# Performance work log

Measured on AMD Instinct MI355X. Metric: run time of the kernel, lower is better.

Reference implementation:

```python
import jax, jax.numpy as jnp
import numpy as np

B, F, D, K = 4096, 1, 256, 65536

def setup_inputs() -> dict:
    key = jax.random.key(0)
    k1, k2, k3 = jax.random.split(key, 3)
    xhat_BFD = jax.random.normal(k1, (B, F, D), dtype=jnp.float32)
    x_BD = jax.random.normal(k2, (B * F, D), dtype=jnp.float32)
    centroids = jax.random.normal(k3, (K, D), dtype=jnp.float32)
    return {"xhat_BFD": xhat_BFD, "x_BD": x_BD, "centroids": centroids}

def reference(xhat_BFD, x_BD, centroids):
    c_sq_K = jnp.sum(centroids * centroids, axis=-1)            # [K]
    dists_BK = c_sq_K[None, :] - 2.0 * (x_BD @ centroids.T)     # [B*F, K] (GEMM-based distances)
    codes_B = jnp.argmin(dists_BK, axis=-1)                      # [B*F]
    quant_x_BD = centroids[codes_B]                              # embedding lookup of winners
    Bb, Ff, Dd = xhat_BFD.shape
    xhat_next = quant_x_BD.reshape(Bb, Ff, Dd)
    codes_BF = codes_B.reshape(Bb, Ff)
    return xhat_next, codes_BF
```

## Files before the change

### kernel.cpp

```cpp
#include <hip/hip_runtime.h>
#include <hip/hip_bf16.h>
#include <math.h>


#define DDIM 256
#define QTILE 128
#define STSZ 8192
#define QCAP 48
#define F16_MINN 6.103515625e-5f

typedef __attribute__((ext_vector_type(8))) _Float16 half8;
typedef __attribute__((ext_vector_type(4))) _Float16 half4;
typedef __attribute__((ext_vector_type(4))) float f32x4;

__device__ __forceinline__ void gl_lds16(const void* g, void* l) {
  __builtin_amdgcn_global_load_lds((const __attribute__((address_space(1))) void*)g,
                                   (__attribute__((address_space(3))) void*)l, 16, 0, 0);
}

__device__ __forceinline__ unsigned fkey(float d) {
  unsigned ud = __float_as_uint(d);
  return ud ^ (((int)ud < 0) ? 0xFFFFFFFFu : 0x80000000u);
}

__global__ void initctl_kernel(unsigned* __restrict__ ctl) {
  if (threadIdx.x < 64) ctl[threadIdx.x] = 0u;
}

__global__ __launch_bounds__(256) void splitc_kernel(const float* __restrict__ in,
                                                     _Float16* __restrict__ o0,
                                                     float* __restrict__ c_sq) {
  int i = blockIdx.x * 256 + threadIdx.x;
  int lane = (int)threadIdx.x & 63;
  float4 v = ((const float4*)in)[i];
  float vv[4] = {v.x, v.y, v.z, v.w};
  half4 h0;
#pragma unroll
  for (int e = 0; e < 4; ++e)
    h0[e] = (fabsf(vv[e]) < F16_MINN) ? (_Float16)0.f : (_Float16)vv[e];
  *(half4*)(o0 + (size_t)i * 4) = h0;
  float s = fmaf(v.x, v.x, fmaf(v.y, v.y, fmaf(v.z, v.z, v.w * v.w)));
#pragma unroll
  for (int off = 32; off > 0; off >>= 1) s += __shfl_down(s, off, 64);
  if (lane == 0) c_sq[i >> 6] = s;
}

__global__ __launch_bounds__(256) void splitx_kernel(const float* __restrict__ in,
                                                     _Float16* __restrict__ o0, int n4) {
  int i = blockIdx.x * 256 + threadIdx.x;
  if (i >= n4) return;
  float4 v = ((const float4*)in)[i];
  float vv[4] = {v.x, v.y, v.z, v.w};
  half4 h0;
#pragma unroll
  for (int e = 0; e < 4; ++e)
    h0[e] = (fabsf(vv[e]) < F16_MINN) ? (_Float16)0.f : (_Float16)vv[e];
  *(half4*)(o0 + (size_t)i * 4) = h0;
}

__global__ __launch_bounds__(256) void cmax_kernel(const float* __restrict__ c_sq,
                                                   unsigned* __restrict__ ctl) {
  __shared__ float red[4];
  int t = blockIdx.x * 256 + (int)threadIdx.x;
  float4 v = ((const float4*)c_sq)[t];
  float m = fmaxf(fmaxf(v.x, v.y), fmaxf(v.z, v.w));
#pragma unroll
  for (int off = 32; off > 0; off >>= 1) m = fmaxf(m, __shfl_down(m, off, 64));
  int lane = (int)threadIdx.x & 63, w = (int)threadIdx.x >> 6;
  if (lane == 0) red[w] = m;
  __syncthreads();
  if (threadIdx.x == 0) {
    m = fmaxf(fmaxf(red[0], red[1]), fmaxf(red[2], red[3]));
    atomicMax(&ctl[32], __float_as_uint(m));
  }
}

__global__ __launch_bounds__(1024) void scan_kernel(
    const _Float16* __restrict__ x0, const _Float16* __restrict__ c0,
    const float* __restrict__ c_sq, float* __restrict__ dm) {
  __shared__ __align__(16) _Float16 As0[32768];

  const int kc = blockIdx.x, qb = blockIdx.y;
  const int tid = (int)threadIdx.x;
  const int lane = tid & 63, w = tid >> 6;
  const int col = lane & 15, quad = lane >> 4;
  const int qrow0 = qb * QTILE;

#pragma unroll
  for (int i = 0; i < 4; ++i) {
    int u = i * 1024 + tid;
    int q = u & 127, s = u >> 7;
    gl_lds16(x0 + (size_t)(qrow0 + q) * DDIM + s * 8, As0 + (size_t)u * 8);
  }
  __syncthreads();

  for (int ct = 0; ct < STSZ / 512; ++ct) {
    const int cbase = kc * STSZ + ct * 512 + w * 32;
    f32x4 acc[2][8];
#pragma unroll
    for (int cm = 0; cm < 2; ++cm)
#pragma unroll
      for (int qn = 0; qn < 8; ++qn) acc[cm][qn] = (f32x4)0.0f;

#pragma unroll 2
    for (int kt = 0; kt < 8; ++kt) {
      const int k0 = kt * 32;
      half8 cf[2];
#pragma unroll
      for (int cm = 0; cm < 2; ++cm)
        cf[cm] = *(const half8*)(c0 + (size_t)(cbase + cm * 16 + col) * DDIM + k0 + quad * 8);
#pragma unroll
      for (int qn = 0; qn < 8; ++qn) {
        half8 qf = *(const half8*)(As0 + (size_t)(((kt * 4 + quad) * QTILE) + qn * 16 + col) * 8);
#pragma unroll
        for (int cm = 0; cm < 2; ++cm)
          acc[cm][qn] = __builtin_amdgcn_mfma_f32_16x16x32_f16(cf[cm], qf, acc[cm][qn], 0, 0, 0);
      }
    }

    f32x4 csv[2];
#pragma unroll
    for (int cm = 0; cm < 2; ++cm)
      csv[cm] = *(const f32x4*)(c_sq + cbase + cm * 16 + quad * 4);
    const int grp = kc * (STSZ / 32) + ct * 16 + w;
    float* dmg = dm + (size_t)grp * 4096 + qrow0;
#pragma unroll
    for (int qn = 0; qn < 8; ++qn) {
      float mq = INFINITY;
#pragma unroll
      for (int cm = 0; cm < 2; ++cm)
#pragma unroll
        for (int rg = 0; rg < 4; ++rg)
          mq = fminf(mq, fmaf(-2.0f, acc[cm][qn][rg], csv[cm][rg]));
      mq = fminf(mq, __shfl_xor(mq, 16, 64));
      mq = fminf(mq, __shfl_xor(mq, 32, 64));
      if (quad == 0) dmg[qn * 16 + col] = mq;
    }
  }
}

__global__ __launch_bounds__(256) void pmin_kernel(const float* __restrict__ dm,
                                                   float* __restrict__ pm) {
  int qc = blockIdx.x & 15, gc = blockIdx.x >> 4;
  int q = qc * 256 + (int)threadIdx.x;
  float m = INFINITY;
  for (int g = gc * 128; g < gc * 128 + 128; ++g)
    m = fminf(m, dm[(size_t)g * 4096 + q]);
  pm[gc * 4096 + q] = m;
}

__global__ __launch_bounds__(256) void tq_kernel(const float* __restrict__ pm,
                                                 const float* __restrict__ x,
                                                 const unsigned* __restrict__ ctl,
                                                 float* __restrict__ T,
                                                 unsigned* __restrict__ cnt) {
  int q = blockIdx.x * 256 + (int)threadIdx.x;
  float M = INFINITY;
#pragma unroll
  for (int i = 0; i < 16; ++i) M = fminf(M, pm[i * 4096 + q]);
  float xsq = 0.f;
  const float4* xr = (const float4*)(x + (size_t)q * DDIM);
#pragma unroll 8
  for (int i = 0; i < 64; ++i) {
    float4 v = xr[i];
    xsq = fmaf(v.x, v.x, fmaf(v.y, v.y, fmaf(v.z, v.z, fmaf(v.w, v.w, xsq))));
  }
  float cmaxsq = __uint_as_float(ctl[32]);
  T[q] = M + 0.0078125f * sqrtf(xsq * cmaxsq) + 1.0f;
  cnt[q] = 0u;
}

__global__ __launch_bounds__(256) void emit_kernel(const float* __restrict__ dm,
                                                   const float* __restrict__ T,
                                                   unsigned short* __restrict__ cand,
                                                   unsigned* __restrict__ cnt) {
  int qc = blockIdx.x & 15, gc = blockIdx.x >> 4;
  int q = qc * 256 + (int)threadIdx.x;
  float t = T[q];
  for (int g = gc * 128; g < gc * 128 + 128; ++g)
    if (dm[(size_t)g * 4096 + q] <= t) {
      unsigned slot = atomicAdd(&cnt[q], 1u);
      if (slot < QCAP) cand[(size_t)q * QCAP + slot] = (unsigned short)g;
    }
}

__global__ __launch_bounds__(256) void rescore_final_kernel(
    const unsigned short* __restrict__ cand, const unsigned* __restrict__ cnt,
    const float* __restrict__ x, const float* __restrict__ cent,
    const float* __restrict__ c_sq, float* __restrict__ out) {
  int q = blockIdx.x * 4 + ((int)threadIdx.x >> 6);
  int lane = (int)threadIdx.x & 63;
  unsigned n = cnt[q];
  unsigned long long best = 0xFFFFFFFFFFFFFFFFull;
  if (n >= 1 && n <= QCAP) {
    int dh = (lane & 1) * 128;
    const float4* xr = (const float4*)(x + (size_t)q * DDIM + dh);
    for (unsigned sl = 0; sl < n; ++sl) {
      int g = (int)cand[(size_t)q * QCAP + sl];
      int c = g * 32 + (lane >> 1);
      const float4* cr = (const float4*)(cent + (size_t)c * DDIM + dh);
      float s = 0.f;
#pragma unroll
      for (int i = 0; i < 32; ++i) {
        float4 a = xr[i], bb = cr[i];
        s = fmaf(a.x, bb.x, fmaf(a.y, bb.y, fmaf(a.z, bb.z, fmaf(a.w, bb.w, s))));
      }
      s += __shfl_xor(s, 1, 64);
      float d = (lane & 1) ? INFINITY : fmaf(-2.0f, s, c_sq[c]);
      unsigned long long pkv = ((unsigned long long)fkey(d) << 32) | (unsigned)c;
      if (pkv < best) best = pkv;
    }
  } else {
    const float4* xr = (const float4*)(x + (size_t)q * DDIM);
    for (int c = lane; c < 65536; c += 64) {
      const float4* cr = (const float4*)(cent + (size_t)c * DDIM);
      float s = 0.f;
#pragma unroll 16
      for (int i = 0; i < 64; ++i) {
        float4 a = xr[i], bb = cr[i];
        s = fmaf(a.x, bb.x, fmaf(a.y, bb.y, fmaf(a.z, bb.z, fmaf(a.w, bb.w, s))));
      }
      float d = fmaf(-2.0f, s, c_sq[c]);
      unsigned long long pkv = ((unsigned long long)fkey(d) << 32) | (unsigned)c;
      if (pkv < best) best = pkv;
    }
  }
#pragma unroll
  for (int off = 1; off < 64; off <<= 1) {
    unsigned long long o = __shfl_xor(best, off, 64);
    if (o < best) best = o;
  }
  int idx = (int)(unsigned)(best & 0xFFFFFFFFu);
  float4 v = ((const float4*)cent)[(size_t)idx * 64 + lane];
  ((float4*)out)[(size_t)q * 64 + lane] = v;
  if (lane == 0) out[(size_t)4096 * DDIM + q] = (float)idx;
}

extern "C" void kernel_launch(void* const* d_in, const int* in_sizes, int n_in,
                              void* d_out, int out_size, void* d_ws, size_t ws_size,
                              hipStream_t stream) {
  const float* x    = (const float*)d_in[1];
  const float* cent = (const float*)d_in[2];
  float* out = (float*)d_out;
  char* ws = (char*)d_ws;

  const size_t OFF_C0   = 0;
  const size_t OFF_X0   = 33554432;
  const size_t OFF_CSQ  = 35651584;
  const size_t OFF_CTL  = 35913728;
  const size_t OFF_DM   = 35913984;
  const size_t OFF_PM   = 69468416;
  const size_t OFF_T    = 69730560;
  const size_t OFF_CNT  = 69746944;
  const size_t OFF_CAND = 69763328;
  const size_t NEED     = 72089600;
  if (ws_size < NEED) return;

  _Float16* c0 = (_Float16*)(ws + OFF_C0);
  _Float16* x0 = (_Float16*)(ws + OFF_X0);
  float* c_sq = (float*)(ws + OFF_CSQ);
  unsigned* ctl = (unsigned*)(ws + OFF_CTL);
  float* dm = (float*)(ws + OFF_DM);
  float* pm = (float*)(ws + OFF_PM);
  float* T  = (float*)(ws + OFF_T);
  unsigned* cnt = (unsigned*)(ws + OFF_CNT);
  unsigned short* cand = (unsigned short*)(ws + OFF_CAND);

  initctl_kernel<<<1, 64, 0, stream>>>(ctl);
  splitc_kernel<<<16384, 256, 0, stream>>>(cent, c0, c_sq);
  splitx_kernel<<<1024, 256, 0, stream>>>(x, x0, 4096 * 256 / 4);
  cmax_kernel<<<64, 256, 0, stream>>>(c_sq, ctl);
  scan_kernel<<<dim3(8, 32), 1024, 0, stream>>>(x0, c0, c_sq, dm);
  pmin_kernel<<<256, 256, 0, stream>>>(dm, pm);
  tq_kernel<<<16, 256, 0, stream>>>(pm, x, ctl, T, cnt);
  emit_kernel<<<256, 256, 0, stream>>>(dm, T, cand, cnt);
  rescore_final_kernel<<<1024, 256, 0, stream>>>(cand, cnt, x, cent, c_sq, out);
}
```

Measured before the change: 380.1 us.

## Fuse per-tile min into scan, fold init into splitx, widen rescore to block-per-query

Drops the separate initctl and pmin launches: the control-word reset moves into splitx, and each scan block now keeps a shared-memory running minimum per query and writes one partial minimum per centroid chunk (8 chunks instead of 16). The rescore kernel now assigns a whole 256-thread block to each query, splitting candidates across four waves and combining them through shared memory. This saves two launches and the full re-read of the distance matrix, and gives rescore four times the parallelism, at the cost of extra LDS work in the scan epilogue.

```diff
diff --git a/kernel.cpp b/kernel.cpp
--- a/kernel.cpp
+++ b/kernel.cpp
@@ -21,10 +21,6 @@
 __device__ __forceinline__ unsigned fkey(float d) {
   unsigned ud = __float_as_uint(d);
   return ud ^ (((int)ud < 0) ? 0xFFFFFFFFu : 0x80000000u);
-}
-
-__global__ void initctl_kernel(unsigned* __restrict__ ctl) {
-  if (threadIdx.x < 64) ctl[threadIdx.x] = 0u;
 }
 
 __global__ __launch_bounds__(256) void splitc_kernel(const float* __restrict__ in,
@@ -46,7 +42,9 @@
 }
 
 __global__ __launch_bounds__(256) void splitx_kernel(const float* __restrict__ in,
-                                                     _Float16* __restrict__ o0, int n4) {
+                                                     _Float16* __restrict__ o0, int n4,
+                                                     unsigned* __restrict__ ctl) {
+  if (blockIdx.x == 0 && threadIdx.x < 64) ctl[threadIdx.x] = 0u;
   int i = blockIdx.x * 256 + threadIdx.x;
   if (i >= n4) return;
   float4 v = ((const float4*)in)[i];
@@ -77,8 +75,10 @@
 
 __global__ __launch_bounds__(1024) void scan_kernel(
     const _Float16* __restrict__ x0, const _Float16* __restrict__ c0,
-    const float* __restrict__ c_sq, float* __restrict__ dm) {
+    const float* __restrict__ c_sq, float* __restrict__ dm,
+    float* __restrict__ pm) {
   __shared__ __align__(16) _Float16 As0[32768];
+  __shared__ float pmred[2048];
 
   const int kc = blockIdx.x, qb = blockIdx.y;
   const int tid = (int)threadIdx.x;
@@ -86,6 +86,9 @@
   const int col = lane & 15, quad = lane >> 4;
   const int qrow0 = qb * QTILE;
 
+  pmred[tid] = INFINITY;
+  pmred[tid + 1024] = INFINITY;
+
 #pragma unroll
   for (int i = 0; i < 4; ++i) {
     int u = i * 1024 + tid;
@@ -134,19 +137,21 @@
           mq = fminf(mq, fmaf(-2.0f, acc[cm][qn][rg], csv[cm][rg]));
       mq = fminf(mq, __shfl_xor(mq, 16, 64));
       mq = fminf(mq, __shfl_xor(mq, 32, 64));
-      if (quad == 0) dmg[qn * 16 + col] = mq;
-    }
-  }
-}
-
-__global__ __launch_bounds__(256) void pmin_kernel(const float* __restrict__ dm,
-                                                   float* __restrict__ pm) {
-  int qc = blockIdx.x & 15, gc = blockIdx.x >> 4;
-  int q = qc * 256 + (int)threadIdx.x;
-  float m = INFINITY;
-  for (int g = gc * 128; g < gc * 128 + 128; ++g)
-    m = fminf(m, dm[(size_t)g * 4096 + q]);
-  pm[gc * 4096 + q] = m;
+      if (quad == 0) {
+        dmg[qn * 16 + col] = mq;
+        const int pi = w * 128 + qn * 16 + col;
+        pmred[pi] = fminf(pmred[pi], mq);
+      }
+    }
+  }
+
+  __syncthreads();
+  if (tid < 128) {
+    float m = INFINITY;
+#pragma unroll
+    for (int i = 0; i < 16; ++i) m = fminf(m, pmred[i * 128 + tid]);
+    pm[(size_t)kc * 4096 + qrow0 + tid] = m;
+  }
 }
 
 __global__ __launch_bounds__(256) void tq_kernel(const float* __restrict__ pm,
@@ -157,7 +162,7 @@
   int q = blockIdx.x * 256 + (int)threadIdx.x;
   float M = INFINITY;
 #pragma unroll
-  for (int i = 0; i < 16; ++i) M = fminf(M, pm[i * 4096 + q]);
+  for (int i = 0; i < 8; ++i) M = fminf(M, pm[i * 4096 + q]);
   float xsq = 0.f;
   const float4* xr = (const float4*)(x + (size_t)q * DDIM);
 #pragma unroll 8
@@ -188,14 +193,15 @@
     const unsigned short* __restrict__ cand, const unsigned* __restrict__ cnt,
     const float* __restrict__ x, const float* __restrict__ cent,
     const float* __restrict__ c_sq, float* __restrict__ out) {
-  int q = blockIdx.x * 4 + ((int)threadIdx.x >> 6);
-  int lane = (int)threadIdx.x & 63;
-  unsigned n = cnt[q];
+  __shared__ unsigned long long red[4];
+  const int q = blockIdx.x;
+  const int w = (int)threadIdx.x >> 6, lane = (int)threadIdx.x & 63;
+  const unsigned n = cnt[q];
   unsigned long long best = 0xFFFFFFFFFFFFFFFFull;
   if (n >= 1 && n <= QCAP) {
     int dh = (lane & 1) * 128;
     const float4* xr = (const float4*)(x + (size_t)q * DDIM + dh);
-    for (unsigned sl = 0; sl < n; ++sl) {
+    for (unsigned sl = (unsigned)w; sl < n; sl += 4) {
       int g = (int)cand[(size_t)q * QCAP + sl];
       int c = g * 32 + (lane >> 1);
       const float4* cr = (const float4*)(cent + (size_t)c * DDIM + dh);
@@ -212,7 +218,7 @@
     }
   } else {
     const float4* xr = (const float4*)(x + (size_t)q * DDIM);
-    for (int c = lane; c < 65536; c += 64) {
+    for (int c = (w << 6) + lane; c < 65536; c += 256) {
       const float4* cr = (const float4*)(cent + (size_t)c * DDIM);
       float s = 0.f;
 #pragma unroll 16
@@ -230,10 +236,20 @@
     unsigned long long o = __shfl_xor(best, off, 64);
     if (o < best) best = o;
   }
-  int idx = (int)(unsigned)(best & 0xFFFFFFFFu);
-  float4 v = ((const float4*)cent)[(size_t)idx * 64 + lane];
-  ((float4*)out)[(size_t)q * 64 + lane] = v;
-  if (lane == 0) out[(size_t)4096 * DDIM + q] = (float)idx;
+  if (lane == 0) red[w] = best;
+  __syncthreads();
+  if (w == 0) {
+    unsigned long long b = red[lane & 3];
+#pragma unroll
+    for (int off = 1; off < 4; off <<= 1) {
+      unsigned long long o = __shfl_xor(b, off, 64);
+      if (o < b) b = o;
+    }
+    int idx = (int)(unsigned)(b & 0xFFFFFFFFu);
+    float4 v = ((const float4*)cent)[(size_t)idx * 64 + lane];
+    ((float4*)out)[(size_t)q * 64 + lane] = v;
+    if (lane == 0) out[(size_t)4096 * DDIM + q] = (float)idx;
+  }
 }
 
 extern "C" void kernel_launch(void* const* d_in, const int* in_sizes, int n_in,
@@ -266,13 +282,11 @@
   unsigned* cnt = (unsigned*)(ws + OFF_CNT);
   unsigned short* cand = (unsigned short*)(ws + OFF_CAND);
 
-  initctl_kernel<<<1, 64, 0, stream>>>(ctl);
   splitc_kernel<<<16384, 256, 0, stream>>>(cent, c0, c_sq);
-  splitx_kernel<<<1024, 256, 0, stream>>>(x, x0, 4096 * 256 / 4);
+  splitx_kernel<<<1024, 256, 0, stream>>>(x, x0, 4096 * 256 / 4, ctl);
   cmax_kernel<<<64, 256, 0, stream>>>(c_sq, ctl);
-  scan_kernel<<<dim3(8, 32), 1024, 0, stream>>>(x0, c0, c_sq, dm);
-  pmin_kernel<<<256, 256, 0, stream>>>(dm, pm);
+  scan_kernel<<<dim3(8, 32), 1024, 0, stream>>>(x0, c0, c_sq, dm, pm);
   tq_kernel<<<16, 256, 0, stream>>>(pm, x, ctl, T, cnt);
   emit_kernel<<<256, 256, 0, stream>>>(dm, T, cand, cnt);
-  rescore_final_kernel<<<1024, 256, 0, stream>>>(cand, cnt, x, cent, c_sq, out);
-}
+  rescore_final_kernel<<<4096, 256, 0, stream>>>(cand, cnt, x, cent, c_sq, out);
+}
```

New measurement: 355.2 us. -6.5%, faster.
